# Performance work log

Measured on AMD Instinct MI355X. Metric: run time of the kernel, lower is better.

## Reference

```python
import jax, jax.numpy as jnp
import numpy as np

N = 50000
E = 800000
IN_C = 128
OUT_C = 64   # per-head dim C == out_channels (concat=False)
HEADS = 4
FFN_H = 256
SQRT_HALF = 0.70710678
LN_EPS = 1e-7


def setup_inputs() -> dict:
    key = jax.random.key(0)
    ks = jax.random.split(key, 16)
    s = 0.05
    return {
        "x": jax.random.normal(ks[0], (N, IN_C), jnp.float32),
        "edge_index": jax.random.randint(ks[1], (2, E), 0, N, jnp.int64),
        # GATv2 params
        "Wl": jax.random.normal(ks[2], (HEADS * OUT_C, IN_C), jnp.float32) * s,
        "Wr": jax.random.normal(ks[3], (HEADS * OUT_C, IN_C), jnp.float32) * s,
        "att": jax.random.normal(ks[4], (HEADS, OUT_C), jnp.float32) * s,
        "bias": jax.random.normal(ks[5], (OUT_C,), jnp.float32) * s,
        # block linears
        "W_affn1": jax.random.normal(ks[6], (OUT_C, IN_C), jnp.float32) * s,
        "b_affn1": jnp.zeros((OUT_C,), jnp.float32),
        "W_affn2": jax.random.normal(ks[7], (OUT_C, OUT_C), jnp.float32) * s,
        "b_affn2": jnp.zeros((OUT_C,), jnp.float32),
        # layernorms
        "g1": jnp.ones((IN_C,), jnp.float32),
        "beta1": jnp.zeros((IN_C,), jnp.float32),
        "g2": jnp.ones((OUT_C,), jnp.float32),
        "beta2": jnp.zeros((OUT_C,), jnp.float32),
        # FFN: out_channels -> 256 -> out_channels
        "W1": jax.random.normal(ks[8], (FFN_H, OUT_C), jnp.float32) * s,
        "b1": jnp.zeros((FFN_H,), jnp.float32),
        "W2": jax.random.normal(ks[9], (OUT_C, FFN_H), jnp.float32) * s,
        "b2": jnp.zeros((OUT_C,), jnp.float32),
    }


def _ln(v, g, b):
    m = jnp.mean(v, axis=-1, keepdims=True)
    var = jnp.var(v, axis=-1, keepdims=True)
    return (v - m) * jax.lax.rsqrt(var + LN_EPS) * g + b


def reference(x, edge_index, Wl, Wr, att, bias, W_affn1, b_affn1,
              W_affn2, b_affn2, g1, beta1, g2, beta2, W1, b1, W2, b2):
    n = x.shape[0]
    H, C = att.shape
    dst = edge_index[0]
    src = edge_index[1]

    x_res = x @ W_affn1.T + b_affn1            # (N, OUT_C)
    h = _ln(x, g1, beta1)                      # (N, IN_C)

    # GATv2 attention (concat=False, no self loops)
    x_l = (h @ Wl.T).reshape(n, H, C)
    x_r = (h @ Wr.T).reshape(n, H, C)
    x_j = x_r[src]                             # (E, H, C)
    e = jax.nn.leaky_relu(x_l[dst] + x_j, 0.2) # (E, H, C)
    logits = jnp.einsum('ehc,hc->eh', e, att)  # (E, H)

    # segment softmax over destination nodes (per head)
    mx = jax.ops.segment_max(logits, dst, num_segments=n)
    ex = jnp.exp(logits - mx[dst])
    den = jax.ops.segment_sum(ex, dst, num_segments=n)
    alpha = ex / (den[dst] + 1e-16)            # (E, H)

    agg = jnp.zeros((n, H, C), x.dtype).at[dst].add(x_j * alpha[..., None])
    attn_out = jnp.mean(agg, axis=1) + bias    # (N, OUT_C)

    out = SQRT_HALF * attn_out + SQRT_HALF * x_res

    # FFN half of the block (pre-LN, matching the attention half's structure)
    h2 = _ln(out, g2, beta2)
    f = jax.nn.relu(h2 @ W1.T + b1) @ W2.T + b2
    res2 = out @ W_affn2.T + b_affn2
    return SQRT_HALF * f + SQRT_HALF * res2
```

## Files before the change

kernel.cpp:

```cpp
#include <hip/hip_runtime.h>
#include <hip/hip_bf16.h>
#include <hip/hip_fp16.h>
#include <math.h>


#define SQRT_HALF 0.70710678f
#define LN_EPS 1e-7f

typedef __attribute__((ext_vector_type(8))) short bf16x8;
typedef __attribute__((ext_vector_type(4))) float f32x4;
typedef _Float16 f16x2 __attribute__((ext_vector_type(2)));

__device__ __forceinline__ float wave_reduce_sum64(float v) {
  #pragma unroll
  for (int m = 1; m < 64; m <<= 1) v += __shfl_xor(v, m, 64);
  return v;
}
__device__ __forceinline__ unsigned short f2bf_bits(float f) {
  __hip_bfloat16 b = __float2bfloat16(f);
  return *reinterpret_cast<unsigned short*>(&b);
}
__device__ __forceinline__ unsigned int pack2bf(float lo, float hi) {
  return (unsigned int)f2bf_bits(lo) | ((unsigned int)f2bf_bits(hi) << 16);
}
__device__ __forceinline__ __half2 u2h(unsigned int u) {
  union { unsigned int u; __half2 h; } c; c.u = u; return c.h;
}
__device__ __forceinline__ __half2 h2abs(__half2 v) {
  union { __half2 h; unsigned int u; } c; c.h = v;
  c.u &= 0x7fff7fffu;
  return c.h;
}
__device__ __forceinline__ f16x2 h2f(__half2 h) {
  union { __half2 h; f16x2 f; } c; c.h = h; return c.f;
}
__device__ __forceinline__ __half2 shflx_h2(__half2 v, int m) {
  union { unsigned int u; __half2 h; } c; c.h = v;
  c.u = (unsigned int)__shfl_xor((int)c.u, m, 64);
  return c.h;
}
__device__ __forceinline__ float dpp_xor1_add(float p) {
  int t = __builtin_amdgcn_update_dpp(0, __float_as_int(p), 0xB1, 0xf, 0xf, true);
  return p + __int_as_float(t);
}
__device__ __forceinline__ float dpp_xor2_add(float p) {
  int t = __builtin_amdgcn_update_dpp(0, __float_as_int(p), 0x4E, 0xf, 0xf, true);
  return p + __int_as_float(t);
}

#define NCHUNK 128
#define WMAX 12800

__global__ __launch_bounds__(256) void prep_kernel(
    const float* __restrict__ x, const float* __restrict__ g1,
    const float* __restrict__ beta1, __hip_bfloat16* __restrict__ h,
    __hip_bfloat16* __restrict__ xbf,
    const float* __restrict__ wl, const float* __restrict__ wr,
    const float* __restrict__ wa1, const float* __restrict__ w1,
    const float* __restrict__ w2, const float* __restrict__ wa2,
    const float* __restrict__ b2c, const float* __restrict__ ba2,
    const float* __restrict__ att,
    __hip_bfloat16* __restrict__ wcat, __hip_bfloat16* __restrict__ wa1b,
    __hip_bfloat16* __restrict__ w1b, __hip_bfloat16* __restrict__ w2b,
    __hip_bfloat16* __restrict__ wa2b, __half* __restrict__ att2,
    float* __restrict__ biasc,
    const int* __restrict__ ei, unsigned int* __restrict__ counts,
    int E_, int n, int W, int S, int gLN) {
  __shared__ unsigned int bins[WMAX];
  int bx = blockIdx.x, tid = threadIdx.x;
  if (bx < gLN) {
    int node = bx * 4 + (tid >> 6);
    if (node >= n) return;
    int lane = tid & 63;
    const float* xr = x + (size_t)node * 128;
    float a = xr[lane], c = xr[lane + 64];
    float s1 = wave_reduce_sum64(a + c) * (1.f / 128.f);
    float s2 = wave_reduce_sum64(a * a + c * c) * (1.f / 128.f);
    float inv = rsqrtf(s2 - s1 * s1 + LN_EPS);
    __hip_bfloat16* hr = h + (size_t)node * 128;
    hr[lane]      = __float2bfloat16((a - s1) * inv * g1[lane] + beta1[lane]);
    hr[lane + 64] =
        __float2bfloat16((c - s1) * inv * g1[lane + 64] + beta1[lane + 64]);
    __hip_bfloat16* xbr = xbf + (size_t)node * 128;
    xbr[lane]      = __float2bfloat16(a);
    xbr[lane + 64] = __float2bfloat16(c);
  } else if (bx < gLN + NCHUNK) {
    int c = bx - gLN;
    for (int i = tid; i < W; i += 256) bins[i] = 0u;
    __syncthreads();
    int e0 = c * S, e1 = c * S + S;
    if (e1 > E_) e1 = E_;
    for (int e = e0 + tid; e < e1; e += 256) {
      int dst = ei[e];
      atomicAdd(&bins[dst >> 2], 1u << ((dst & 3) * 8));
    }
    __syncthreads();
    unsigned int* crow = counts + (size_t)c * W;
    for (int i = tid; i < W; i += 256) crow[i] = bins[i];
  } else {
    int gid = (bx - gLN - NCHUNK) * 256 + tid;
    for (int i = gid; i < 110912; i += 64 * 256) {
      if (i < 65536) {
        wcat[i] = __float2bfloat16(i < 32768 ? wl[i] : wr[i - 32768]);
      } else if (i < 73728) {
        int j = i - 65536; wa1b[j] = __float2bfloat16(wa1[j]);
      } else if (i < 90112) {
        int j = i - 73728; w1b[j] = __float2bfloat16(w1[j]);
      } else if (i < 106496) {
        int j = i - 90112; w2b[j] = __float2bfloat16(w2[j]);
      } else if (i < 110592) {
        int j = i - 106496; wa2b[j] = __float2bfloat16(wa2[j]);
      } else if (i < 110848) {
        int j = i - 110592; att2[j] = __float2half(att[j]);
      } else {
        int j = i - 110848; biasc[j] = SQRT_HALF * (b2c[j] + ba2[j]);
      }
    }
  }
}

__global__ __launch_bounds__(256) void scan_kernel(
    unsigned int* __restrict__ counts, unsigned int* __restrict__ degw,
    int W) {
  int gid = blockIdx.x * 256 + threadIdx.x;
  int w = gid >> 3, g = gid & 7;
  if (w >= W) return;
  unsigned int v[16];
  unsigned int s = 0;
  #pragma unroll
  for (int i = 0; i < 16; ++i) {
    v[i] = counts[(size_t)(g * 16 + i) * W + w];
    s += v[i];
  }
  unsigned int run = s;
  #pragma unroll
  for (int off = 1; off < 8; off <<= 1) {
    unsigned int u = __shfl_up(run, off, 64);
    if (g >= off) run += u;
  }
  unsigned int base = run - s;
  #pragma unroll
  for (int i = 0; i < 16; ++i) {
    counts[(size_t)(g * 16 + i) * W + w] = base;
    base += v[i];
  }
  if (g == 7) degw[w] = base;
}

__global__ __launch_bounds__(256) void mfma_pre(
    const short* __restrict__ h, const short* __restrict__ xbf,
    const short* __restrict__ wcat, const short* __restrict__ wa1b,
    const float* __restrict__ ba1, __half* __restrict__ xlxr,
    float* __restrict__ xres, const int* __restrict__ ei,
    const unsigned int* __restrict__ counts, unsigned short* __restrict__ ell,
    int E_, int n, int W, int S, int ntiles) {
  __shared__ unsigned int bins[WMAX];
  int tid = threadIdx.x;
  int wv = tid >> 6, l = tid & 63;
  int lane_m = l & 15, kg = l >> 4;
  if (blockIdx.y < 4) {
    int bn = blockIdx.y * 128;
    bf16x8 wf[4][8];
    const short* wp = wcat + (size_t)(bn + lane_m) * 128 + kg * 8;
    #pragma unroll
    for (int ks = 0; ks < 4; ++ks)
      #pragma unroll
      for (int ct = 0; ct < 8; ++ct)
        wf[ks][ct] = *(const bf16x8*)(wp + (size_t)ct * 16 * 128 + ks * 32);
    for (int t = blockIdx.x; t < ntiles; t += gridDim.x) {
      int node = t * 64 + wv * 16 + lane_m;
      int nodec = node < n ? node : n - 1;
      const short* ap = h + (size_t)nodec * 128 + kg * 8;
      f32x4 acc[8] = {};
      #pragma unroll
      for (int ks = 0; ks < 4; ++ks) {
        bf16x8 af = *(const bf16x8*)(ap + ks * 32);
        #pragma unroll
        for (int ct = 0; ct < 8; ++ct)
          acc[ct] = __builtin_amdgcn_mfma_f32_16x16x32_bf16(
              wf[ks][ct], af, acc[ct], 0, 0, 0);
      }
      if (node < n) {
        #pragma unroll
        for (int ct = 0; ct < 8; ++ct) {
          int col = bn + ct * 16 + kg * 4;
          ushort4 s;
          s.x = __half_as_ushort(__float2half(acc[ct][0]));
          s.y = __half_as_ushort(__float2half(acc[ct][1]));
          s.z = __half_as_ushort(__float2half(acc[ct][2]));
          s.w = __half_as_ushort(__float2half(acc[ct][3]));
          *(ushort4*)((unsigned short*)xlxr + (size_t)node * 512 + col) = s;
        }
      }
    }
  } else if (blockIdx.y == 4) {
    bf16x8 wf[4][4];
    const short* wp = wa1b + (size_t)lane_m * 128 + kg * 8;
    #pragma unroll
    for (int ks = 0; ks < 4; ++ks)
      #pragma unroll
      for (int ct = 0; ct < 4; ++ct)
        wf[ks][ct] = *(const bf16x8*)(wp + (size_t)ct * 16 * 128 + ks * 32);
    float4 bias4[4];
    #pragma unroll
    for (int ct = 0; ct < 4; ++ct)
      bias4[ct] = *(const float4*)(ba1 + ct * 16 + kg * 4);
    for (int t = blockIdx.x; t < ntiles; t += gridDim.x) {
      int node = t * 64 + wv * 16 + lane_m;
      int nodec = node < n ? node : n - 1;
      const short* ap = xbf + (size_t)nodec * 128 + kg * 8;
      f32x4 acc[4] = {};
      #pragma unroll
      for (int ks = 0; ks < 4; ++ks) {
        bf16x8 af = *(const bf16x8*)(ap + ks * 32);
        #pragma unroll
        for (int ct = 0; ct < 4; ++ct)
          acc[ct] = __builtin_amdgcn_mfma_f32_16x16x32_bf16(
              wf[ks][ct], af, acc[ct], 0, 0, 0);
      }
      if (node < n) {
        #pragma unroll
        for (int ct = 0; ct < 4; ++ct) {
          int col = ct * 16 + kg * 4;
          *(float4*)(xres + (size_t)node * 64 + col) = make_float4(
              acc[ct][0] + ((const float*)&bias4[ct])[0],
              acc[ct][1] + ((const float*)&bias4[ct])[1],
              acc[ct][2] + ((const float*)&bias4[ct])[2],
              acc[ct][3] + ((const float*)&bias4[ct])[3]);
        }
      }
    }
  } else {
    int c = blockIdx.x;
    if (c >= NCHUNK) return;
    for (int i = tid; i < W; i += 256) bins[i] = 0u;
    __syncthreads();
    int e0 = c * S, e1 = c * S + S;
    if (e1 > E_) e1 = E_;
    const unsigned int* cbase = counts + (size_t)c * W;
    for (int e = e0 + tid; e < e1; e += 256) {
      int dst = ei[e], src = ei[E_ + e];
      int sh = (dst & 3) * 8;
      unsigned int old = atomicAdd(&bins[dst >> 2], 1u << sh);
      int local = (int)((old >> sh) & 0xffu);
      int base = (int)((cbase[dst >> 2] >> sh) & 0xffu);
      int slot = base + local;
      if (slot < 64) ell[((size_t)dst << 6) + slot] = (unsigned short)src;
    }
  }
}

__global__ __launch_bounds__(256) void fused_edge_kernel(
    const unsigned int* __restrict__ degw, const unsigned short* __restrict__ ell,
    const __half* __restrict__ xlxr,
    const __half* __restrict__ att2, const float* __restrict__ xres,
    const float* __restrict__ bias, const float* __restrict__ g2,
    const float* __restrict__ b2, __hip_bfloat16* __restrict__ outb,
    __hip_bfloat16* __restrict__ h2, int n) {
  int node = blockIdx.x * 4 + (threadIdx.x >> 6);
  if (node >= n) return;
  int lane = threadIdx.x & 63;
  int half_ = lane >> 5;
  int hl = lane & 31;
  int q = hl & 7;
  int off8 = (hl >> 3) * 64 + q * 8;
  uint4 va = *(const uint4*)(xlxr + (size_t)node * 512 + off8);
  __half2 xa2[4] = {u2h(va.x), u2h(va.y), u2h(va.z), u2h(va.w)};
  uint4 vt = *(const uint4*)(att2 + off8);
  const __half2 c06 = __float2half2_rn(0.6f);
  const __half2 c04 = __float2half2_rn(0.4f);
  __half2 at6[4], at4[4];
  #pragma unroll
  for (int c = 0; c < 4; ++c) {
    __half2 a = u2h(((const unsigned int*)&vt)[c]);
    at6[c] = __hmul2(c06, a);
    at4[c] = __hmul2(c04, a);
  }
  int d = (int)((degw[node >> 2] >> ((node & 3) * 8)) & 0xffu);
  d = d < 64 ? d : 64;
  float den = 0.f;
  __half2 ac2[4] = {__float2half2_rn(0.f), __float2half2_rn(0.f),
                    __float2half2_rn(0.f), __float2half2_rn(0.f)};
  if (d > 0) {
    int dm1 = d - 1;
    int dpairs = d >> 1;
    const __half* xrbase = xlxr + 256 + off8;
    int myidx = (int)ell[((size_t)node << 6) + (lane <= dm1 ? lane : dm1)];
    int srcA = __shfl(myidx, half_ <= dm1 ? half_ : dm1, 64);
    int srcB = __shfl(myidx, 2 + half_ <= dm1 ? 2 + half_ : dm1, 64);
    uint4 vbA = *(const uint4*)(xrbase + (size_t)srcA * 512);
    uint4 vbB = *(const uint4*)(xrbase + (size_t)srcB * 512);
    #pragma unroll 2
    for (int k = 0; k < dpairs; ++k) {
      int jC = 2 * k + 4 + half_;
      jC = jC <= dm1 ? jC : dm1;
      int srcC = __shfl(myidx, jC, 64);
      uint4 vbC = *(const uint4*)(xrbase + (size_t)srcC * 512);
      __half2 xb2[4] = {u2h(vbA.x), u2h(vbA.y), u2h(vbA.z), u2h(vbA.w)};
      float p = 0.f;
      #pragma unroll
      for (int c = 0; c < 4; ++c) {
        __half2 s = __hadd2(xa2[c], xb2[c]);
        p = __builtin_amdgcn_fdot2(h2f(at6[c]), h2f(s), p, false);
        p = __builtin_amdgcn_fdot2(h2f(at4[c]), h2f(h2abs(s)), p, false);
      }
      p = dpp_xor1_add(p);
      p = dpp_xor2_add(p);
      p += __shfl_xor(p, 4, 64);
      float ex = __expf(p);
      den += ex;
      __half2 ex2 = __float2half2_rn(ex);
      #pragma unroll
      for (int c = 0; c < 4; ++c) ac2[c] = __hfma2(ex2, xb2[c], ac2[c]);
      vbA = vbB; vbB = vbC;
    }
    if (d & 1) {
      __half2 xb2[4] = {u2h(vbA.x), u2h(vbA.y), u2h(vbA.z), u2h(vbA.w)};
      float p = 0.f;
      #pragma unroll
      for (int c = 0; c < 4; ++c) {
        __half2 s = __hadd2(xa2[c], xb2[c]);
        p = __builtin_amdgcn_fdot2(h2f(at6[c]), h2f(s), p, false);
        p = __builtin_amdgcn_fdot2(h2f(at4[c]), h2f(h2abs(s)), p, false);
      }
      p = dpp_xor1_add(p);
      p = dpp_xor2_add(p);
      p += __shfl_xor(p, 4, 64);
      float ex = (half_ == 0) ? __expf(p) : 0.f;
      den += ex;
      __half2 ex2 = __float2half2_rn(ex);
      #pragma unroll
      for (int c = 0; c < 4; ++c) ac2[c] = __hfma2(ex2, xb2[c], ac2[c]);
    }
  }
  #pragma unroll
  for (int c = 0; c < 4; ++c) ac2[c] = __hadd2(ac2[c], shflx_h2(ac2[c], 32));
  den += __shfl_xor(den, 32, 64);
  float inv = 1.f / (den + 1e-16f);
  __half2 inv2 = __float2half2_rn(inv);
  #pragma unroll
  for (int c = 0; c < 4; ++c) {
    __half2 a = __hmul2(ac2[c], inv2);
    a = __hadd2(a, shflx_h2(a, 8));
    a = __hadd2(a, shflx_h2(a, 16));
    ac2[c] = a;
  }
  float acf[8];
  #pragma unroll
  for (int c = 0; c < 4; ++c) {
    acf[2 * c]     = __low2float(ac2[c]);
    acf[2 * c + 1] = __high2float(ac2[c]);
  }
  float o[8];
  {
    float4 bi0 = *(const float4*)(bias + q * 8);
    float4 bi1 = *(const float4*)(bias + q * 8 + 4);
    float4 xr0 = *(const float4*)(xres + (size_t)node * 64 + q * 8);
    float4 xr1 = *(const float4*)(xres + (size_t)node * 64 + q * 8 + 4);
    float bi[8] = {bi0.x, bi0.y, bi0.z, bi0.w, bi1.x, bi1.y, bi1.z, bi1.w};
    float xr[8] = {xr0.x, xr0.y, xr0.z, xr0.w, xr1.x, xr1.y, xr1.z, xr1.w};
    #pragma unroll
    for (int c = 0; c < 8; ++c)
      o[c] = SQRT_HALF * (acf[c] * 0.25f + bi[c] + xr[c]);
  }
  float s1 = 0.f, s2 = 0.f;
  #pragma unroll
  for (int c = 0; c < 8; ++c) { s1 += o[c]; s2 += o[c] * o[c]; }
  s1 = dpp_xor1_add(s1); s2 = dpp_xor1_add(s2);
  s1 = dpp_xor2_add(s1); s2 = dpp_xor2_add(s2);
  s1 += __shfl_xor(s1, 4, 64); s2 += __shfl_xor(s2, 4, 64);
  float mean = s1 * (1.f / 64.f);
  float var = s2 * (1.f / 64.f) - mean * mean;
  float rinv = rsqrtf(var + LN_EPS);
  if (lane < 8) {
    float4 g0 = *(const float4*)(g2 + q * 8);
    float4 g1v = *(const float4*)(g2 + q * 8 + 4);
    float4 e0 = *(const float4*)(b2 + q * 8);
    float4 e1 = *(const float4*)(b2 + q * 8 + 4);
    float gg[8] = {g0.x, g0.y, g0.z, g0.w, g1v.x, g1v.y, g1v.z, g1v.w};
    float ee[8] = {e0.x, e0.y, e0.z, e0.w, e1.x, e1.y, e1.z, e1.w};
    uint4 ov, hv;
    ov.x = pack2bf(o[0], o[1]); ov.y = pack2bf(o[2], o[3]);
    ov.z = pack2bf(o[4], o[5]); ov.w = pack2bf(o[6], o[7]);
    float t[8];
    #pragma unroll
    for (int c = 0; c < 8; ++c)
      t[c] = (o[c] - mean) * rinv * gg[c] + ee[c];
    hv.x = pack2bf(t[0], t[1]); hv.y = pack2bf(t[2], t[3]);
    hv.z = pack2bf(t[4], t[5]); hv.w = pack2bf(t[6], t[7]);
    *(uint4*)((unsigned short*)outb + (size_t)node * 64 + q * 8) = ov;
    *(uint4*)((unsigned short*)h2 + (size_t)node * 64 + q * 8) = hv;
  }
}

__global__ __launch_bounds__(256) void ffn_fused(
    const __hip_bfloat16* __restrict__ h2, const __hip_bfloat16* __restrict__ outb,
    const __hip_bfloat16* __restrict__ w1b, const __hip_bfloat16* __restrict__ w2b,
    const __hip_bfloat16* __restrict__ wa2b, const float* __restrict__ b1,
    const float* __restrict__ biasc, float* __restrict__ out,
    int n, int ntiles) {
  __shared__ unsigned short lds[4][16][280];
  int tid = threadIdx.x;
  int wv = tid >> 6, l = tid & 63;
  int lane_m = l & 15, kg = l >> 4;
  bf16x8 wf1[2][16];
  #pragma unroll
  for (int ks = 0; ks < 2; ++ks)
    #pragma unroll
    for (int ct = 0; ct < 16; ++ct)
      wf1[ks][ct] = *(const bf16x8*)(
          (const short*)w1b + (size_t)(ct * 16 + lane_m) * 64 + ks * 32 + kg * 8);
  for (int t = blockIdx.x; t < ntiles; t += gridDim.x) {
    int node = t * 64 + wv * 16 + lane_m;
    int nodec = node < n ? node : n - 1;
    const short* hp = (const short*)h2 + (size_t)nodec * 64 + kg * 8;
    bf16x8 af1[2];
    af1[0] = *(const bf16x8*)(hp);
    af1[1] = *(const bf16x8*)(hp + 32);
    f32x4 acc1[16] = {};
    #pragma unroll
    for (int ks = 0; ks < 2; ++ks)
      #pragma unroll
      for (int ct = 0; ct < 16; ++ct)
        acc1[ct] = __builtin_amdgcn_mfma_f32_16x16x32_bf16(
            wf1[ks][ct], af1[ks], acc1[ct], 0, 0, 0);
    #pragma unroll
    for (int ct = 0; ct < 16; ++ct) {
      float4 bb = *(const float4*)(b1 + ct * 16 + kg * 4);
      ushort4 s;
      s.x = f2bf_bits(fmaxf(acc1[ct][0] + bb.x, 0.f));
      s.y = f2bf_bits(fmaxf(acc1[ct][1] + bb.y, 0.f));
      s.z = f2bf_bits(fmaxf(acc1[ct][2] + bb.z, 0.f));
      s.w = f2bf_bits(fmaxf(acc1[ct][3] + bb.w, 0.f));
      *(ushort4*)&lds[wv][lane_m][ct * 16 + kg * 4] = s;
    }
    f32x4 acc2[4] = {};
    #pragma unroll
    for (int ks = 0; ks < 8; ++ks) {
      bf16x8 af2 = *(const bf16x8*)&lds[wv][lane_m][ks * 32 + kg * 8];
      #pragma unroll
      for (int ct = 0; ct < 4; ++ct) {
        bf16x8 wf2 = *(const bf16x8*)(
            (const short*)w2b + (size_t)(ct * 16 + lane_m) * 256 + ks * 32 + kg * 8);
        acc2[ct] = __builtin_amdgcn_mfma_f32_16x16x32_bf16(
            wf2, af2, acc2[ct], 0, 0, 0);
      }
    }
    const short* op = (const short*)outb + (size_t)nodec * 64 + kg * 8;
    #pragma unroll
    for (int ks = 0; ks < 2; ++ks) {
      bf16x8 afo = *(const bf16x8*)(op + ks * 32);
      #pragma unroll
      for (int ct = 0; ct < 4; ++ct) {
        bf16x8 wfo = *(const bf16x8*)(
            (const short*)wa2b + (size_t)(ct * 16 + lane_m) * 64 + ks * 32 + kg * 8);
        acc2[ct] = __builtin_amdgcn_mfma_f32_16x16x32_bf16(
            wfo, afo, acc2[ct], 0, 0, 0);
      }
    }
    if (node < n) {
      #pragma unroll
      for (int ct = 0; ct < 4; ++ct) {
        float4 bc = *(const float4*)(biasc + ct * 16 + kg * 4);
        float4 v = make_float4(SQRT_HALF * acc2[ct][0] + bc.x,
                               SQRT_HALF * acc2[ct][1] + bc.y,
                               SQRT_HALF * acc2[ct][2] + bc.z,
                               SQRT_HALF * acc2[ct][3] + bc.w);
        *(float4*)(out + (size_t)node * 64 + ct * 16 + kg * 4) = v;
      }
    }
  }
}

extern "C" void kernel_launch(void* const* d_in, const int* in_sizes, int n_in,
                              void* d_out, int out_size, void* d_ws,
                              size_t ws_size, hipStream_t stream) {
  const float* x       = (const float*)d_in[0];
  const int*   ei      = (const int*)d_in[1];
  const float* Wl      = (const float*)d_in[2];
  const float* Wr      = (const float*)d_in[3];
  const float* att     = (const float*)d_in[4];
  const float* bias    = (const float*)d_in[5];
  const float* W_affn1 = (const float*)d_in[6];
  const float* b_affn1 = (const float*)d_in[7];
  const float* W_affn2 = (const float*)d_in[8];
  const float* b_affn2 = (const float*)d_in[9];
  const float* g1      = (const float*)d_in[10];
  const float* beta1   = (const float*)d_in[11];
  const float* g2      = (const float*)d_in[12];
  const float* beta2   = (const float*)d_in[13];
  const float* W1      = (const float*)d_in[14];
  const float* b1      = (const float*)d_in[15];
  const float* W2      = (const float*)d_in[16];
  const float* b2      = (const float*)d_in[17];
  int n  = in_sizes[0] / 128;
  int E_ = in_sizes[1] / 2;

  int W = (n + 3) >> 2;
  int S = (E_ + NCHUNK - 1) / NCHUNK;
  int ntiles = (n + 63) / 64;
  int gLN = (n + 3) / 4;

  float* ws = (float*)d_ws;
  size_t o_xlxr = 0;
  size_t o_h    = o_xlxr + (size_t)n * 256;
  size_t o_xbf  = o_h + (size_t)n * 64;
  size_t o_xres = o_xbf + (size_t)n * 64;
  size_t o_h2   = o_xres + (size_t)n * 64;
  size_t o_outb = o_h2 + (size_t)n * 32;
  size_t o_w    = o_outb + (size_t)n * 32;
  __half* xlxr         = (__half*)(ws + o_xlxr);
  __hip_bfloat16* h    = (__hip_bfloat16*)(ws + o_h);
  __hip_bfloat16* xbf  = (__hip_bfloat16*)(ws + o_xbf);
  float* xres          = ws + o_xres;
  __hip_bfloat16* h2   = (__hip_bfloat16*)(ws + o_h2);
  __hip_bfloat16* outb = (__hip_bfloat16*)(ws + o_outb);
  __hip_bfloat16* wcat = (__hip_bfloat16*)(ws + o_w);
  __hip_bfloat16* wa1b = (__hip_bfloat16*)(ws + o_w + 32768);
  __hip_bfloat16* w1b  = (__hip_bfloat16*)(ws + o_w + 36864);
  __hip_bfloat16* w2b  = (__hip_bfloat16*)(ws + o_w + 45056);
  __hip_bfloat16* wa2b = (__hip_bfloat16*)(ws + o_w + 53248);
  __half* att2         = (__half*)(ws + o_w + 55296);
  float* biasc         = ws + o_w + 55424;
  size_t o_cnt = o_w + 55488;
  unsigned int* counts = (unsigned int*)(ws + o_cnt);
  unsigned int* degw   = counts + (size_t)NCHUNK * W;
  unsigned short* ell  = (unsigned short*)(degw + W);

  prep_kernel<<<gLN + NCHUNK + 64, 256, 0, stream>>>(
      x, g1, beta1, h, xbf, Wl, Wr, W_affn1, W1, W2, W_affn2, b2, b_affn2,
      att, wcat, wa1b, w1b, w2b, wa2b, att2, biasc, ei, counts,
      E_, n, W, S, gLN);

  scan_kernel<<<(W * 8 + 255) / 256, 256, 0, stream>>>(counts, degw, W);

  mfma_pre<<<dim3(NCHUNK, 6), 256, 0, stream>>>(
      (const short*)h, (const short*)xbf, (const short*)wcat,
      (const short*)wa1b, b_affn1, xlxr, xres, ei, counts, ell,
      E_, n, W, S, ntiles);

  fused_edge_kernel<<<(n + 3) / 4, 256, 0, stream>>>(
      degw, ell, xlxr, att2, xres, bias, g2, beta2, outb, h2, n);

  ffn_fused<<<ntiles, 256, 0, stream>>>(
      h2, outb, w1b, w2b, wa2b, b1, biasc, (float*)d_out, n, ntiles);
}
```

Before: 199.2 us.

## Replace per-node counting sort with two-level bucket sort into ELL

Edge-to-ELL construction now runs as a two-level radix sort. Edges are first counted and scattered into 256-node buckets, which shrinks the per-chunk histograms and the scan from about 12800 words to about 196. A new per-bucket kernel then builds each bucket's ELL rows and packed degrees in shared memory and writes them out with coalesced stores. This cuts the large LDS footprint and histogram traffic of the old scheme, at the cost of two extra kernel launches and an intermediate record array written and read once.

```diff
diff --git a/kernel.cpp b/kernel.cpp
--- a/kernel.cpp
+++ b/kernel.cpp
@@ -49,7 +49,6 @@
 }
 
 #define NCHUNK 128
-#define WMAX 12800
 
 __global__ __launch_bounds__(256) void prep_kernel(
     const float* __restrict__ x, const float* __restrict__ g1,
@@ -65,8 +64,8 @@
     __hip_bfloat16* __restrict__ wa2b, __half* __restrict__ att2,
     float* __restrict__ biasc,
     const int* __restrict__ ei, unsigned int* __restrict__ counts,
-    int E_, int n, int W, int S, int gLN) {
-  __shared__ unsigned int bins[WMAX];
+    int E_, int n, int NBUK, int S, int gLN) {
+  __shared__ unsigned int bins[256];
   int bx = blockIdx.x, tid = threadIdx.x;
   if (bx < gLN) {
     int node = bx * 4 + (tid >> 6);
@@ -86,17 +85,14 @@
     xbr[lane + 64] = __float2bfloat16(c);
   } else if (bx < gLN + NCHUNK) {
     int c = bx - gLN;
-    for (int i = tid; i < W; i += 256) bins[i] = 0u;
+    bins[tid] = 0u;
     __syncthreads();
     int e0 = c * S, e1 = c * S + S;
     if (e1 > E_) e1 = E_;
-    for (int e = e0 + tid; e < e1; e += 256) {
-      int dst = ei[e];
-      atomicAdd(&bins[dst >> 2], 1u << ((dst & 3) * 8));
-    }
+    for (int e = e0 + tid; e < e1; e += 256)
+      atomicAdd(&bins[ei[e] >> 8], 1u);
     __syncthreads();
-    unsigned int* crow = counts + (size_t)c * W;
-    for (int i = tid; i < W; i += 256) crow[i] = bins[i];
+    if (tid < NBUK) counts[(size_t)c * NBUK + tid] = bins[tid];
   } else {
     int gid = (bx - gLN - NCHUNK) * 256 + tid;
     for (int i = gid; i < 110912; i += 64 * 256) {
@@ -119,32 +115,51 @@
   }
 }
 
-__global__ __launch_bounds__(256) void scan_kernel(
-    unsigned int* __restrict__ counts, unsigned int* __restrict__ degw,
-    int W) {
-  int gid = blockIdx.x * 256 + threadIdx.x;
-  int w = gid >> 3, g = gid & 7;
-  if (w >= W) return;
-  unsigned int v[16];
+__global__ __launch_bounds__(256) void scanA_kernel(
+    unsigned int* __restrict__ counts, unsigned int* __restrict__ totals,
+    int NBUK) {
+  int b = blockIdx.x * 4 + (threadIdx.x >> 6);
+  if (b >= NBUK) return;
+  int lane = threadIdx.x & 63;
+  unsigned int a0 = counts[(size_t)(2 * lane) * NBUK + b];
+  unsigned int a1 = counts[(size_t)(2 * lane + 1) * NBUK + b];
+  unsigned int ps = a0 + a1;
+  unsigned int run = ps;
+  #pragma unroll
+  for (int off = 1; off < 64; off <<= 1) {
+    unsigned int u = __shfl_up(run, off, 64);
+    if (lane >= off) run += u;
+  }
+  unsigned int excl = run - ps;
+  counts[(size_t)(2 * lane) * NBUK + b] = excl;
+  counts[(size_t)(2 * lane + 1) * NBUK + b] = excl + a0;
+  if (lane == 63) totals[b] = run;
+}
+
+__global__ void scanB_kernel(const unsigned int* __restrict__ totals,
+                             unsigned int* __restrict__ bucketbase, int NBUK) {
+  int lane = threadIdx.x & 63;
+  unsigned int v[4];
   unsigned int s = 0;
   #pragma unroll
-  for (int i = 0; i < 16; ++i) {
-    v[i] = counts[(size_t)(g * 16 + i) * W + w];
+  for (int i = 0; i < 4; ++i) {
+    int b = lane * 4 + i;
+    v[i] = (b < NBUK) ? totals[b] : 0u;
     s += v[i];
   }
   unsigned int run = s;
   #pragma unroll
-  for (int off = 1; off < 8; off <<= 1) {
+  for (int off = 1; off < 64; off <<= 1) {
     unsigned int u = __shfl_up(run, off, 64);
-    if (g >= off) run += u;
+    if (lane >= off) run += u;
   }
   unsigned int base = run - s;
   #pragma unroll
-  for (int i = 0; i < 16; ++i) {
-    counts[(size_t)(g * 16 + i) * W + w] = base;
+  for (int i = 0; i < 4; ++i) {
+    int b = lane * 4 + i;
+    if (b < NBUK) bucketbase[b] = base;
     base += v[i];
   }
-  if (g == 7) degw[w] = base;
 }
 
 __global__ __launch_bounds__(256) void mfma_pre(
@@ -152,9 +167,11 @@
     const short* __restrict__ wcat, const short* __restrict__ wa1b,
     const float* __restrict__ ba1, __half* __restrict__ xlxr,
     float* __restrict__ xres, const int* __restrict__ ei,
-    const unsigned int* __restrict__ counts, unsigned short* __restrict__ ell,
-    int E_, int n, int W, int S, int ntiles) {
-  __shared__ unsigned int bins[WMAX];
+    const unsigned int* __restrict__ counts,
+    const unsigned int* __restrict__ bucketbase,
+    unsigned int* __restrict__ recs,
+    int E_, int n, int NBUK, int S, int ntiles) {
+  __shared__ unsigned int bins[256];
   int tid = threadIdx.x;
   int wv = tid >> 6, l = tid & 63;
   int lane_m = l & 15, kg = l >> 4;
@@ -233,20 +250,55 @@
   } else {
     int c = blockIdx.x;
     if (c >= NCHUNK) return;
-    for (int i = tid; i < W; i += 256) bins[i] = 0u;
+    bins[tid] = 0u;
     __syncthreads();
     int e0 = c * S, e1 = c * S + S;
     if (e1 > E_) e1 = E_;
-    const unsigned int* cbase = counts + (size_t)c * W;
+    const unsigned int* cpref = counts + (size_t)c * NBUK;
     for (int e = e0 + tid; e < e1; e += 256) {
       int dst = ei[e], src = ei[E_ + e];
-      int sh = (dst & 3) * 8;
-      unsigned int old = atomicAdd(&bins[dst >> 2], 1u << sh);
-      int local = (int)((old >> sh) & 0xffu);
-      int base = (int)((cbase[dst >> 2] >> sh) & 0xffu);
-      int slot = base + local;
-      if (slot < 64) ell[((size_t)dst << 6) + slot] = (unsigned short)src;
-    }
+      int b = dst >> 8;
+      unsigned int pos = atomicAdd(&bins[b], 1u);
+      unsigned int off = bucketbase[b] + cpref[b] + pos;
+      recs[off] = ((unsigned int)(dst & 255) << 16) | (unsigned int)src;
+    }
+  }
+}
+
+__global__ __launch_bounds__(256) void bucket_kernel(
+    const unsigned int* __restrict__ recs,
+    const unsigned int* __restrict__ bucketbase,
+    const unsigned int* __restrict__ totals,
+    unsigned short* __restrict__ ell, unsigned int* __restrict__ degw,
+    int n) {
+  __shared__ unsigned int bins[256];
+  __shared__ unsigned short ellb[256 * 64];
+  int b = blockIdx.x, tid = threadIdx.x;
+  bins[tid] = 0u;
+  __syncthreads();
+  unsigned int start = bucketbase[b];
+  unsigned int nrec = totals[b];
+  for (unsigned int i = tid; i < nrec; i += 256) {
+    unsigned int r = recs[start + i];
+    int dlow = (int)(r >> 16);
+    unsigned int pos = atomicAdd(&bins[dlow], 1u);
+    if (pos < 64) ellb[(dlow << 6) + pos] = (unsigned short)(r & 0xffffu);
+  }
+  __syncthreads();
+  int node0 = b << 8;
+  int nn = n - node0;
+  nn = nn < 256 ? nn : 256;
+  int nquad = nn * 16;
+  ushort4* gq = (ushort4*)(ell + ((size_t)node0 << 6));
+  const ushort4* lq = (const ushort4*)ellb;
+  for (int qd = tid; qd < nquad; qd += 256) gq[qd] = lq[qd];
+  int nw = (nn + 3) >> 2;
+  for (int w = tid; w < nw; w += 256) {
+    unsigned int d0 = bins[4 * w + 0], d1 = bins[4 * w + 1];
+    unsigned int d2 = bins[4 * w + 2], d3 = bins[4 * w + 3];
+    d0 = d0 < 64u ? d0 : 64u; d1 = d1 < 64u ? d1 : 64u;
+    d2 = d2 < 64u ? d2 : 64u; d3 = d3 < 64u ? d3 : 64u;
+    degw[(node0 >> 2) + w] = d0 | (d1 << 8) | (d2 << 16) | (d3 << 24);
   }
 }
 
@@ -496,7 +548,7 @@
   int n  = in_sizes[0] / 128;
   int E_ = in_sizes[1] / 2;
 
-  int W = (n + 3) >> 2;
+  int NBUK = (n + 255) >> 8;
   int S = (E_ + NCHUNK - 1) / NCHUNK;
   int ntiles = (n + 63) / 64;
   int gLN = (n + 3) / 4;
@@ -522,22 +574,29 @@
   __hip_bfloat16* wa2b = (__hip_bfloat16*)(ws + o_w + 53248);
   __half* att2         = (__half*)(ws + o_w + 55296);
   float* biasc         = ws + o_w + 55424;
-  size_t o_cnt = o_w + 55488;
-  unsigned int* counts = (unsigned int*)(ws + o_cnt);
-  unsigned int* degw   = counts + (size_t)NCHUNK * W;
-  unsigned short* ell  = (unsigned short*)(degw + W);
+  size_t o_srt = o_w + 55488;
+  unsigned int* counts     = (unsigned int*)(ws + o_srt);
+  unsigned int* totals     = counts + (size_t)NCHUNK * NBUK;
+  unsigned int* bucketbase = totals + NBUK;
+  unsigned int* degw       = bucketbase + NBUK;
+  unsigned int* recs       = degw + ((n + 3) >> 2);
+  unsigned short* ell      = (unsigned short*)(recs + E_);
 
   prep_kernel<<<gLN + NCHUNK + 64, 256, 0, stream>>>(
       x, g1, beta1, h, xbf, Wl, Wr, W_affn1, W1, W2, W_affn2, b2, b_affn2,
       att, wcat, wa1b, w1b, w2b, wa2b, att2, biasc, ei, counts,
-      E_, n, W, S, gLN);
-
-  scan_kernel<<<(W * 8 + 255) / 256, 256, 0, stream>>>(counts, degw, W);
+      E_, n, NBUK, S, gLN);
+
+  scanA_kernel<<<(NBUK + 3) / 4, 256, 0, stream>>>(counts, totals, NBUK);
+  scanB_kernel<<<1, 64, 0, stream>>>(totals, bucketbase, NBUK);
 
   mfma_pre<<<dim3(NCHUNK, 6), 256, 0, stream>>>(
       (const short*)h, (const short*)xbf, (const short*)wcat,
-      (const short*)wa1b, b_affn1, xlxr, xres, ei, counts, ell,
-      E_, n, W, S, ntiles);
+      (const short*)wa1b, b_affn1, xlxr, xres, ei, counts, bucketbase, recs,
+      E_, n, NBUK, S, ntiles);
+
+  bucket_kernel<<<NBUK, 256, 0, stream>>>(
+      recs, bucketbase, totals, ell, degw, n);
 
   fused_edge_kernel<<<(n + 3) / 4, 256, 0, stream>>>(
       degw, ell, xlxr, att2, xres, bias, g2, beta2, outb, h2, n);
```

Measured after the change: 187.6 us. 1.06x faster.
